# Performance work log

Measured on AMD Instinct MI355X. Metric: run time of the kernel, lower is better.

## Reference

```python
import jax, jax.numpy as jnp
import numpy as np

QK_DIM = 1024
V_DIM = 1024
NUM_HEADS = 16
B, L = 4, 2048


def setup_inputs() -> dict:
    key = jax.random.key(0)
    ks = jax.random.split(key, 12)
    s_in = 1.0 / np.sqrt(QK_DIM)
    inp = {
        "q": jax.random.normal(ks[0], (B, L, QK_DIM), jnp.float32),
        "k": jax.random.normal(ks[1], (B, L, QK_DIM), jnp.float32),
        "v": jax.random.normal(ks[2], (B, L, V_DIM), jnp.float32),
        "Wq": jax.random.uniform(ks[3], (QK_DIM, QK_DIM), jnp.float32, -s_in, s_in),
        "bq": jnp.zeros((QK_DIM,), jnp.float32),
        "Wk": jax.random.uniform(ks[4], (QK_DIM, QK_DIM), jnp.float32, -s_in, s_in),
        "bk": jnp.zeros((QK_DIM,), jnp.float32),
        "Wv": jax.random.uniform(ks[5], (V_DIM, V_DIM), jnp.float32, -s_in, s_in),
        "bv": jnp.zeros((V_DIM,), jnp.float32),
        "Wo": jax.random.uniform(ks[6], (V_DIM, V_DIM), jnp.float32, -s_in, s_in),
        "bo": jnp.zeros((V_DIM,), jnp.float32),
        "offset": jnp.float32(0.0),
    }
    return inp


def _split_heads(x, n_heads):
    b, l, d = x.shape
    return x.reshape(b, l, n_heads, d // n_heads).transpose(0, 2, 1, 3)  # [B,H,L,Dh]


def reference(q, k, v, Wq, bq, Wk, bk, Wv, bv, Wo, bo, offset):
    # in-projections (nn.Linear: x @ W.T + b; here W stored as [in,out])
    q = q @ Wq + bq
    k = k @ Wk + bk
    v = v @ Wv + bv
    scale = (QK_DIM // NUM_HEADS) ** (-0.5)
    q = q * scale
    qh = _split_heads(q, NUM_HEADS)  # [B,H,L,Dh]
    kh = _split_heads(k, NUM_HEADS)
    vh = _split_heads(v, NUM_HEADS)
    scores = jnp.einsum("bhqd,bhkd->bhqk", qh, kh) + offset
    A = jax.nn.softmax(scores, axis=-1)  # attn_dropout is identity in eval
    out = jnp.einsum("bhqk,bhkd->bhqd", A, vh)
    out = out.transpose(0, 2, 1, 3).reshape(B, L, V_DIM)  # merge heads
    out = out @ Wo + bo  # out projection; seq_dropout identity in eval
    return out
```

## Files before the change

kernel.cpp:

```cpp
#include <hip/hip_runtime.h>
#include <hip/hip_bf16.h>
#include <stdint.h>

typedef __bf16 bf16;
typedef __bf16 bf16x8 __attribute__((ext_vector_type(8)));
typedef __bf16 bf16x4v __attribute__((ext_vector_type(4)));
typedef float f32x4 __attribute__((ext_vector_type(4)));
typedef uint32_t u32;
typedef u32 u32x2 __attribute__((ext_vector_type(2)));

__device__ __forceinline__ void gld_lds16(const void* g, void* l) {
  __builtin_amdgcn_global_load_lds(
      (const __attribute__((address_space(1))) void*)g,
      (__attribute__((address_space(3))) void*)l, 16, 0, 0);
}

__device__ __forceinline__ f32x4 mfma16(bf16x8 a, bf16x8 b, f32x4 c) {
  return __builtin_amdgcn_mfma_f32_16x16x32_bf16(a, b, c, 0, 0, 0);
}

__device__ __forceinline__ u32 cvtpk_bf16(float lo, float hi) {
  u32 r;
  asm("v_cvt_pk_bf16_f32 %0, %1, %2" : "=v"(r) : "v"(lo), "v"(hi));
  return r;
}

__device__ __forceinline__ float fexp2(float x) {
#if __has_builtin(__builtin_amdgcn_exp2f)
  return __builtin_amdgcn_exp2f(x);
#else
  return exp2f(x);
#endif
}

__global__ void cvt3_bf16_k(const float* __restrict__ q, const float* __restrict__ k,
                            const float* __restrict__ v, bf16* __restrict__ qb,
                            bf16* __restrict__ kb, bf16* __restrict__ vb, int n4) {
  int i = blockIdx.x * blockDim.x + threadIdx.x;
  if (i >= n4) return;
  const float* in = (blockIdx.y == 0) ? q : (blockIdx.y == 1) ? k : v;
  bf16* out = (blockIdx.y == 0) ? qb : (blockIdx.y == 1) ? kb : vb;
  f32x4 t = reinterpret_cast<const f32x4*>(in)[i];
  bf16x4v o;
  o[0] = (bf16)t[0]; o[1] = (bf16)t[1]; o[2] = (bf16)t[2]; o[3] = (bf16)t[3];
  reinterpret_cast<bf16x4v*>(out)[i] = o;
}

__global__ void wt_cvt4_k(const float* __restrict__ W0, const float* __restrict__ W1,
                          const float* __restrict__ W2, const float* __restrict__ W3,
                          bf16* __restrict__ T0, bf16* __restrict__ T1,
                          bf16* __restrict__ T2, bf16* __restrict__ T3) {
  const float* W = (blockIdx.z == 0) ? W0 : (blockIdx.z == 1) ? W1
                  : (blockIdx.z == 2) ? W2 : W3;
  bf16* WT = (blockIdx.z == 0) ? T0 : (blockIdx.z == 1) ? T1
            : (blockIdx.z == 2) ? T2 : T3;
  __shared__ float t[32][33];
  int tx = threadIdx.x, ty = threadIdx.y;
  int bx = blockIdx.x * 32, by = blockIdx.y * 32;
#pragma unroll
  for (int j = 0; j < 32; j += 8)
    t[ty + j][tx] = W[(size_t)(by + ty + j) * 1024 + bx + tx];
  __syncthreads();
#pragma unroll
  for (int j = 0; j < 32; j += 8)
    WT[(size_t)(bx + ty + j) * 1024 + by + tx] = (bf16)t[tx][ty + j];
}

template <int OUT_MODE>
__global__ __launch_bounds__(256, 2) void gemm_k(
    const bf16* __restrict__ A, const bf16* __restrict__ WT,
    const float* __restrict__ bias, void* __restrict__ Cout, float scale) {
  constexpr int K = 1024, N = 1024, BM = 128, BK = 64;
  constexpr int NT = K / BK;
  __shared__ char lds[2][2][BM * BK * 2];
  const int lane = threadIdx.x & 63, w = threadIdx.x >> 6;
  const int nwg = gridDim.x;
  int bid = (int)blockIdx.x;
  bid = (bid & 7) * (nwg >> 3) + (bid >> 3);
  const int bn = bid & 7;
  const int bm = bid >> 3;
  const int wm = (w & 1) * 64, wn = (w >> 1) * 64;

  const char* gA = (const char*)(A + (size_t)bm * BM * K);
  const char* gB = (const char*)(WT + (size_t)bn * BM * K);

  auto stage = [&](int buf, int kt) {
    char* lA = lds[buf][0];
    char* lB = lds[buf][1];
#pragma unroll
    for (int i = 0; i < 4; ++i) {
      int row = w * 32 + i * 8 + (lane >> 3);
      size_t rb = (size_t)row * (K * 2) + (size_t)kt * (BK * 2) + (size_t)(lane & 7) * 16;
      gld_lds16(gA + rb, lA + (w * 32 + i * 8) * 128);
      gld_lds16(gB + rb, lB + (w * 32 + i * 8) * 128);
    }
  };

  f32x4 acc[4][4] = {};
  stage(0, 0);
  for (int kt = 0; kt < NT; ++kt) {
    __syncthreads();
    if (kt + 1 < NT) stage((kt + 1) & 1, kt + 1);
    const char* lA = lds[kt & 1][0];
    const char* lB = lds[kt & 1][1];
    bf16x8 af[4][2], bfr[4][2];
#pragma unroll
    for (int mi = 0; mi < 4; ++mi)
#pragma unroll
      for (int c = 0; c < 2; ++c) {
        int row = wm + mi * 16 + (lane & 15);
        int ch = c * 4 + (lane >> 4);
        af[mi][c] = *(const bf16x8*)(lA + row * 128 + ch * 16);
      }
#pragma unroll
    for (int ni = 0; ni < 4; ++ni)
#pragma unroll
      for (int c = 0; c < 2; ++c) {
        int row = wn + ni * 16 + (lane & 15);
        int ch = c * 4 + (lane >> 4);
        bfr[ni][c] = *(const bf16x8*)(lB + row * 128 + ch * 16);
      }
#pragma unroll
    for (int mi = 0; mi < 4; ++mi)
#pragma unroll
      for (int ni = 0; ni < 4; ++ni) {
        acc[mi][ni] = mfma16(af[mi][0], bfr[ni][0], acc[mi][ni]);
        acc[mi][ni] = mfma16(af[mi][1], bfr[ni][1], acc[mi][ni]);
      }
  }

#pragma unroll
  for (int ni = 0; ni < 4; ++ni) {
    int col = bn * 128 + wn + ni * 16 + (lane & 15);
    float bv = bias[col];
    if (OUT_MODE == 0) {
      bf16* out = (bf16*)Cout;
      int h = col >> 6, dh = col & 63;
#pragma unroll
      for (int mi = 0; mi < 4; ++mi)
#pragma unroll
        for (int r = 0; r < 4; ++r) {
          int row = bm * BM + wm + mi * 16 + (lane >> 4) * 4 + r;
          int b = row >> 11, li = row & 2047;
          out[(((size_t)(b * 16 + h) * 2048 + li) << 6) + dh] =
              (bf16)((acc[mi][ni][r] + bv) * scale);
        }
    } else if (OUT_MODE == 1) {
      float* out = (float*)Cout;
#pragma unroll
      for (int mi = 0; mi < 4; ++mi)
#pragma unroll
        for (int r = 0; r < 4; ++r) {
          int row = bm * BM + wm + mi * 16 + (lane >> 4) * 4 + r;
          out[(size_t)row * N + col] = acc[mi][ni][r] + bv;
        }
    } else {
      bf16* out = (bf16*)Cout;
      int h = col >> 6, dh = col & 63;
#pragma unroll
      for (int mi = 0; mi < 4; ++mi)
#pragma unroll
        for (int r = 0; r < 4; ++r) {
          int row = bm * BM + wm + mi * 16 + (lane >> 4) * 4 + r;
          int b = row >> 11, li = row & 2047;
          out[(((size_t)(b * 16 + h) * 64 + dh) << 11) + li] =
              (bf16)((acc[mi][ni][r] + bv) * scale);
        }
    }
  }
}

__global__ __launch_bounds__(256, 3) void attn_mfma_k(
    const bf16* __restrict__ Q, const bf16* __restrict__ Kg,
    const bf16* __restrict__ VT, bf16* __restrict__ AO) {
  constexpr int L = 2048, DH = 64, NT = L / 64;
  __shared__ char ldsK[2][8192];
  __shared__ char ldsVT[2][8192];
  __shared__ char ldsP[4][2][2048];
  const int lane = threadIdx.x & 63, w = threadIdx.x >> 6;
  const int nwg = gridDim.x;
  int bid = (int)blockIdx.x;
  bid = (bid & 7) * (nwg >> 3) + (bid >> 3);
  const int bh = bid >> 4;
  const int q0 = (bid & 15) * 128;
  const int b = bh >> 4, h = bh & 15;
  const int l7 = lane & 7;
  const int q15 = lane & 15, g4 = lane >> 4;
  const int sl = lane >> 3;
  const int sw = l7 ^ sl;

  const bf16* Qbase = Q + ((size_t)bh * L + q0 + w * 32) * DH;
  bf16x8 qf[2][2];
#pragma unroll
  for (int rt = 0; rt < 2; ++rt)
#pragma unroll
    for (int c = 0; c < 2; ++c)
      qf[rt][c] = *(const bf16x8*)(Qbase + (size_t)(rt * 16 + q15) * DH +
                                   (c * 4 + g4) * 8);

  const char* Kp  = (const char*)(Kg + (size_t)bh * L * DH);
  const char* VTp = (const char*)(VT + (size_t)bh * DH * L);

  auto stage = [&](int buf, int kt) {
#pragma unroll
    for (int c = 0; c < 2; ++c) {
      int chunk = w * 2 + c;
      int row = chunk * 8 + sl;
      gld_lds16(Kp + (size_t)kt * 8192 + (size_t)row * 128 + sw * 16,
                ldsK[buf] + chunk * 1024);
      gld_lds16(VTp + (size_t)row * 4096 + (size_t)kt * 128 + sw * 16,
                ldsVT[buf] + chunk * 1024);
    }
  };

  f32x4 o[2][4] = {};
  float lpart[2] = {0.f, 0.f};

  stage(0, 0);
  for (int kt = 0; kt < NT; ++kt) {
    __syncthreads();
    if (kt + 1 < NT) stage((kt + 1) & 1, kt + 1);
    const char* lK  = ldsK[kt & 1];
    const char* lVT = ldsVT[kt & 1];

    bf16x8 kf[4][2];
#pragma unroll
    for (int sub = 0; sub < 4; ++sub)
#pragma unroll
      for (int c = 0; c < 2; ++c) {
        int key = sub * 16 + q15;
        int ch = (c * 4 + g4) ^ l7;
        kf[sub][c] = *(const bf16x8*)(lK + key * 128 + ch * 16);
      }

#pragma unroll
    for (int rt = 0; rt < 2; ++rt) {
      f32x4 s[4];
#pragma unroll
      for (int sub = 0; sub < 4; ++sub) {
        f32x4 acc = {};
        acc = mfma16(kf[sub][0], qf[rt][0], acc);
        acc = mfma16(kf[sub][1], qf[rt][1], acc);
        s[sub] = acc;
      }
#pragma unroll
      for (int sub = 0; sub < 4; ++sub) {
        float p0 = fexp2(s[sub][0]), p1 = fexp2(s[sub][1]);
        float p2 = fexp2(s[sub][2]), p3 = fexp2(s[sub][3]);
        lpart[rt] += (p0 + p1) + (p2 + p3);
        u32x2 pw;
        pw[0] = cvtpk_bf16(p0, p1);
        pw[1] = cvtpk_bf16(p2, p3);
        bf16x4v pv = __builtin_bit_cast(bf16x4v, pw);
        int chs = (2 * sub + (g4 >> 1)) ^ l7;
        *(bf16x4v*)(ldsP[w][rt] + q15 * 128 + chs * 16 + (g4 & 1) * 8) = pv;
      }
    }

    asm volatile("s_waitcnt lgkmcnt(0)" ::: "memory");
    __builtin_amdgcn_sched_barrier(0);

    bf16x8 pf[2][2];
#pragma unroll
    for (int rt = 0; rt < 2; ++rt)
#pragma unroll
      for (int c = 0; c < 2; ++c) {
        int ch = (c * 4 + g4) ^ l7;
        pf[rt][c] = *(const bf16x8*)(ldsP[w][rt] + q15 * 128 + ch * 16);
      }

#pragma unroll
    for (int n = 0; n < 4; ++n) {
      int dim = n * 16 + q15;
      bf16x8 vf[2];
#pragma unroll
      for (int c = 0; c < 2; ++c) {
        int ch = (c * 4 + g4) ^ l7;
        vf[c] = *(const bf16x8*)(lVT + dim * 128 + ch * 16);
      }
#pragma unroll
      for (int rt = 0; rt < 2; ++rt) {
        o[rt][n] = mfma16(pf[rt][0], vf[0], o[rt][n]);
        o[rt][n] = mfma16(pf[rt][1], vf[1], o[rt][n]);
      }
    }
  }

  float lf[2];
#pragma unroll
  for (int rt = 0; rt < 2; ++rt) {
    float v = lpart[rt];
    v += __shfl_xor(v, 16, 64);
    v += __shfl_xor(v, 32, 64);
    lf[rt] = v;
  }

#pragma unroll
  for (int rt = 0; rt < 2; ++rt) {
    float inv[4];
#pragma unroll
    for (int r = 0; r < 4; ++r)
      inv[r] = 1.f / __shfl(lf[rt], g4 * 4 + r, 64);
#pragma unroll
    for (int n = 0; n < 4; ++n) {
      int col = h * 64 + n * 16 + q15;
#pragma unroll
      for (int r = 0; r < 4; ++r) {
        int qrow = q0 + w * 32 + rt * 16 + g4 * 4 + r;
        AO[((size_t)b * L + qrow) * 1024 + col] = (bf16)(o[rt][n][r] * inv[r]);
      }
    }
  }
}

extern "C" void kernel_launch(void* const* d_in, const int* in_sizes, int n_in,
                              void* d_out, int out_size, void* d_ws, size_t ws_size,
                              hipStream_t stream) {
  (void)in_sizes; (void)n_in; (void)out_size;
  const size_t MB = 1u << 20;
  if (ws_size < 73 * MB) return;

  const float* q  = (const float*)d_in[0];
  const float* k  = (const float*)d_in[1];
  const float* v  = (const float*)d_in[2];
  const float* Wq = (const float*)d_in[3];
  const float* bq = (const float*)d_in[4];
  const float* Wk = (const float*)d_in[5];
  const float* bk = (const float*)d_in[6];
  const float* Wv = (const float*)d_in[7];
  const float* bv = (const float*)d_in[8];
  const float* Wo = (const float*)d_in[9];
  const float* bo = (const float*)d_in[10];

  char* ws = (char*)d_ws;
  bf16* qb  = (bf16*)(ws + 0 * MB);
  bf16* kb  = (bf16*)(ws + 16 * MB);
  bf16* vb  = (bf16*)(ws + 32 * MB);
  bf16* Qa  = (bf16*)(ws + 48 * MB);
  bf16* WqT = (bf16*)(ws + 64 * MB);
  bf16* WkT = (bf16*)(ws + 66 * MB);
  bf16* WvT = (bf16*)(ws + 68 * MB);
  bf16* WoT = (bf16*)(ws + 70 * MB);
  bf16* Ka = qb;
  bf16* VTa = kb;
  bf16* AO = vb;

  dim3 tb(32, 8);
  wt_cvt4_k<<<dim3(32, 32, 4), tb, 0, stream>>>(Wq, Wk, Wv, Wo, WqT, WkT, WvT, WoT);

  const int n4 = (4 * 2048 * 1024) / 4;
  cvt3_bf16_k<<<dim3(n4 / 256, 3), 256, 0, stream>>>(q, k, v, qb, kb, vb, n4);

  gemm_k<0><<<512, 256, 0, stream>>>(qb, WqT, bq, (void*)Qa, 0.125f * 1.4426950408889634f);
  gemm_k<0><<<512, 256, 0, stream>>>(kb, WkT, bk, (void*)Ka, 1.0f);
  gemm_k<2><<<512, 256, 0, stream>>>(vb, WvT, bv, (void*)VTa, 1.0f);

  attn_mfma_k<<<1024, 256, 0, stream>>>(Qa, Ka, VTa, AO);

  gemm_k<1><<<512, 256, 0, stream>>>(AO, WoT, bo, d_out, 1.0f);
}
```

Before: 215.9 us.

## Fuse fp32-to-bf16 input conversion into batched QKV projection GEMM

Removes the separate pass that converts q/k/v to bf16. The projection GEMM now loads fp32 activations directly, converts them in registers, and writes them swizzled into LDS. The three Q/K/V projection launches are merged into one launch with a grid y-dimension that selects the operand set. This saves a full read and write of the bf16 activation copies plus two launches. In exchange, the A-tile loads become synchronous register loads instead of async global-to-LDS transfers, which may reduce overlap in the main loop.

```diff
diff --git a/kernel.cpp b/kernel.cpp
--- a/kernel.cpp
+++ b/kernel.cpp
@@ -8,6 +8,7 @@
 typedef float f32x4 __attribute__((ext_vector_type(4)));
 typedef uint32_t u32;
 typedef u32 u32x2 __attribute__((ext_vector_type(2)));
+typedef u32 u32x4 __attribute__((ext_vector_type(4)));
 
 __device__ __forceinline__ void gld_lds16(const void* g, void* l) {
   __builtin_amdgcn_global_load_lds(
@@ -31,19 +32,6 @@
 #else
   return exp2f(x);
 #endif
-}
-
-__global__ void cvt3_bf16_k(const float* __restrict__ q, const float* __restrict__ k,
-                            const float* __restrict__ v, bf16* __restrict__ qb,
-                            bf16* __restrict__ kb, bf16* __restrict__ vb, int n4) {
-  int i = blockIdx.x * blockDim.x + threadIdx.x;
-  if (i >= n4) return;
-  const float* in = (blockIdx.y == 0) ? q : (blockIdx.y == 1) ? k : v;
-  bf16* out = (blockIdx.y == 0) ? qb : (blockIdx.y == 1) ? kb : vb;
-  f32x4 t = reinterpret_cast<const f32x4*>(in)[i];
-  bf16x4v o;
-  o[0] = (bf16)t[0]; o[1] = (bf16)t[1]; o[2] = (bf16)t[2]; o[3] = (bf16)t[3];
-  reinterpret_cast<bf16x4v*>(out)[i] = o;
 }
 
 __global__ void wt_cvt4_k(const float* __restrict__ W0, const float* __restrict__ W1,
@@ -66,10 +54,124 @@
     WT[(size_t)(bx + ty + j) * 1024 + by + tx] = (bf16)t[tx][ty + j];
 }
 
-template <int OUT_MODE>
-__global__ __launch_bounds__(256, 2) void gemm_k(
+__global__ __launch_bounds__(256, 2) void gemmf_k(
+    const float* __restrict__ Aq, const float* __restrict__ Ak, const float* __restrict__ Av,
+    const bf16* __restrict__ WTq, const bf16* __restrict__ WTk, const bf16* __restrict__ WTv,
+    const float* __restrict__ bq, const float* __restrict__ bk, const float* __restrict__ bv,
+    bf16* __restrict__ Qa, bf16* __restrict__ Ka, bf16* __restrict__ VTa, float qscale) {
+  constexpr int K = 1024, BM = 128, BK = 64;
+  constexpr int NT = K / BK;
+  __shared__ char lds[2][2][BM * BK * 2];
+  const int lane = threadIdx.x & 63, w = threadIdx.x >> 6;
+  const int y = blockIdx.y;
+  const float* A   = (y == 0) ? Aq : (y == 1) ? Ak : Av;
+  const bf16* WT   = (y == 0) ? WTq : (y == 1) ? WTk : WTv;
+  const float* bias = (y == 0) ? bq : (y == 1) ? bk : bv;
+  const float scale = (y == 0) ? qscale : 1.0f;
+  const int nwg = gridDim.x;
+  int bid = (int)blockIdx.x;
+  bid = (bid & 7) * (nwg >> 3) + (bid >> 3);
+  const int bn = bid & 7;
+  const int bm = bid >> 3;
+  const int wm = (w & 1) * 64, wn = (w >> 1) * 64;
+  const int l7 = lane & 7, sl = lane >> 3;
+  const int sw = l7 ^ sl;
+
+  const char* gA = (const char*)(A + (size_t)bm * BM * K);
+  const char* gB = (const char*)(WT + (size_t)bn * BM * K);
+
+  auto stage = [&](int buf, int kt) {
+    char* lA = lds[buf][0];
+    char* lB = lds[buf][1];
+#pragma unroll
+    for (int i = 0; i < 4; ++i) {
+      int row = w * 32 + i * 8 + sl;
+      size_t rb = (size_t)row * 2048 + (size_t)kt * 128 + (size_t)l7 * 16;
+      gld_lds16(gB + rb, lB + (w * 32 + i * 8) * 128);
+    }
+#pragma unroll
+    for (int i = 0; i < 4; ++i) {
+      int row = w * 32 + i * 8 + sl;
+      const char* src = gA + (size_t)row * 4096 + (size_t)kt * 256 + (size_t)l7 * 32;
+      f32x4 a0 = *(const f32x4*)src;
+      f32x4 a1 = *(const f32x4*)(src + 16);
+      u32x4 pk;
+      pk[0] = cvtpk_bf16(a0[0], a0[1]);
+      pk[1] = cvtpk_bf16(a0[2], a0[3]);
+      pk[2] = cvtpk_bf16(a1[0], a1[1]);
+      pk[3] = cvtpk_bf16(a1[2], a1[3]);
+      bf16x8 v8 = __builtin_bit_cast(bf16x8, pk);
+      *(bf16x8*)(lA + row * 128 + sw * 16) = v8;
+    }
+  };
+
+  f32x4 acc[4][4] = {};
+  stage(0, 0);
+  for (int kt = 0; kt < NT; ++kt) {
+    __syncthreads();
+    if (kt + 1 < NT) stage((kt + 1) & 1, kt + 1);
+    const char* lA = lds[kt & 1][0];
+    const char* lB = lds[kt & 1][1];
+    bf16x8 af[4][2], bfr[4][2];
+#pragma unroll
+    for (int mi = 0; mi < 4; ++mi)
+#pragma unroll
+      for (int c = 0; c < 2; ++c) {
+        int row = wm + mi * 16 + (lane & 15);
+        int ch = (c * 4 + (lane >> 4)) ^ (lane & 7);
+        af[mi][c] = *(const bf16x8*)(lA + row * 128 + ch * 16);
+      }
+#pragma unroll
+    for (int ni = 0; ni < 4; ++ni)
+#pragma unroll
+      for (int c = 0; c < 2; ++c) {
+        int row = wn + ni * 16 + (lane & 15);
+        int ch = c * 4 + (lane >> 4);
+        bfr[ni][c] = *(const bf16x8*)(lB + row * 128 + ch * 16);
+      }
+#pragma unroll
+    for (int mi = 0; mi < 4; ++mi)
+#pragma unroll
+      for (int ni = 0; ni < 4; ++ni) {
+        acc[mi][ni] = mfma16(af[mi][0], bfr[ni][0], acc[mi][ni]);
+        acc[mi][ni] = mfma16(af[mi][1], bfr[ni][1], acc[mi][ni]);
+      }
+  }
+
+#pragma unroll
+  for (int ni = 0; ni < 4; ++ni) {
+    int col = bn * 128 + wn + ni * 16 + (lane & 15);
+    float bv2 = bias[col];
+    int h = col >> 6, dh = col & 63;
+    if (y != 2) {
+      bf16* out = (y == 0) ? Qa : Ka;
+#pragma unroll
+      for (int mi = 0; mi < 4; ++mi)
+#pragma unroll
+        for (int r = 0; r < 4; ++r) {
+          int row = bm * BM + wm + mi * 16 + (lane >> 4) * 4 + r;
+          int b = row >> 11, li = row & 2047;
+          out[(((size_t)(b * 16 + h) * 2048 + li) << 6) + dh] =
+              (bf16)((acc[mi][ni][r] + bv2) * scale);
+        }
+    } else {
+      bf16* out = VTa;
+#pragma unroll
+      for (int mi = 0; mi < 4; ++mi)
+#pragma unroll
+        for (int r = 0; r < 4; ++r) {
+          int row = bm * BM + wm + mi * 16 + (lane >> 4) * 4 + r;
+          int b = row >> 11, li = row & 2047;
+          out[(((size_t)(b * 16 + h) * 64 + dh) << 11) + li] =
+              (bf16)(acc[mi][ni][r] + bv2);
+        }
+    }
+  }
+}
+
+__global__ __launch_bounds__(256, 2) void gemm_out_k(
     const bf16* __restrict__ A, const bf16* __restrict__ WT,
-    const float* __restrict__ bias, void* __restrict__ Cout, float scale) {
+    const float* __restrict__ bias, float* __restrict__ Cout) {
   constexpr int K = 1024, N = 1024, BM = 128, BK = 64;
   constexpr int NT = K / BK;
   __shared__ char lds[2][2][BM * BK * 2];
@@ -133,40 +235,13 @@
   for (int ni = 0; ni < 4; ++ni) {
     int col = bn * 128 + wn + ni * 16 + (lane & 15);
     float bv = bias[col];
-    if (OUT_MODE == 0) {
-      bf16* out = (bf16*)Cout;
-      int h = col >> 6, dh = col & 63;
-#pragma unroll
-      for (int mi = 0; mi < 4; ++mi)
-#pragma unroll
-        for (int r = 0; r < 4; ++r) {
-          int row = bm * BM + wm + mi * 16 + (lane >> 4) * 4 + r;
-          int b = row >> 11, li = row & 2047;
-          out[(((size_t)(b * 16 + h) * 2048 + li) << 6) + dh] =
-              (bf16)((acc[mi][ni][r] + bv) * scale);
-        }
-    } else if (OUT_MODE == 1) {
-      float* out = (float*)Cout;
-#pragma unroll
-      for (int mi = 0; mi < 4; ++mi)
-#pragma unroll
-        for (int r = 0; r < 4; ++r) {
-          int row = bm * BM + wm + mi * 16 + (lane >> 4) * 4 + r;
-          out[(size_t)row * N + col] = acc[mi][ni][r] + bv;
-        }
-    } else {
-      bf16* out = (bf16*)Cout;
-      int h = col >> 6, dh = col & 63;
-#pragma unroll
-      for (int mi = 0; mi < 4; ++mi)
-#pragma unroll
-        for (int r = 0; r < 4; ++r) {
-          int row = bm * BM + wm + mi * 16 + (lane >> 4) * 4 + r;
-          int b = row >> 11, li = row & 2047;
-          out[(((size_t)(b * 16 + h) * 64 + dh) << 11) + li] =
-              (bf16)((acc[mi][ni][r] + bv) * scale);
-        }
-    }
+#pragma unroll
+    for (int mi = 0; mi < 4; ++mi)
+#pragma unroll
+      for (int r = 0; r < 4; ++r) {
+        int row = bm * BM + wm + mi * 16 + (lane >> 4) * 4 + r;
+        Cout[(size_t)row * N + col] = acc[mi][ni][r] + bv;
+      }
   }
 }
 
@@ -333,29 +408,23 @@
   const float* bo = (const float*)d_in[10];
 
   char* ws = (char*)d_ws;
-  bf16* qb  = (bf16*)(ws + 0 * MB);
-  bf16* kb  = (bf16*)(ws + 16 * MB);
-  bf16* vb  = (bf16*)(ws + 32 * MB);
-  bf16* Qa  = (bf16*)(ws + 48 * MB);
+  bf16* Qa  = (bf16*)(ws + 0 * MB);
+  bf16* Ka  = (bf16*)(ws + 16 * MB);
+  bf16* VTa = (bf16*)(ws + 32 * MB);
+  bf16* AO  = (bf16*)(ws + 48 * MB);
   bf16* WqT = (bf16*)(ws + 64 * MB);
   bf16* WkT = (bf16*)(ws + 66 * MB);
   bf16* WvT = (bf16*)(ws + 68 * MB);
   bf16* WoT = (bf16*)(ws + 70 * MB);
-  bf16* Ka = qb;
-  bf16* VTa = kb;
-  bf16* AO = vb;
 
   dim3 tb(32, 8);
   wt_cvt4_k<<<dim3(32, 32, 4), tb, 0, stream>>>(Wq, Wk, Wv, Wo, WqT, WkT, WvT, WoT);
 
-  const int n4 = (4 * 2048 * 1024) / 4;
-  cvt3_bf16_k<<<dim3(n4 / 256, 3), 256, 0, stream>>>(q, k, v, qb, kb, vb, n4);
-
-  gemm_k<0><<<512, 256, 0, stream>>>(qb, WqT, bq, (void*)Qa, 0.125f * 1.4426950408889634f);
-  gemm_k<0><<<512, 256, 0, stream>>>(kb, WkT, bk, (void*)Ka, 1.0f);
-  gemm_k<2><<<512, 256, 0, stream>>>(vb, WvT, bv, (void*)VTa, 1.0f);
+  gemmf_k<<<dim3(512, 3), 256, 0, stream>>>(
+      q, k, v, WqT, WkT, WvT, bq, bk, bv, Qa, Ka, VTa,
+      0.125f * 1.4426950408889634f);
 
   attn_mfma_k<<<1024, 256, 0, stream>>>(Qa, Ka, VTa, AO);
 
-  gemm_k<1><<<512, 256, 0, stream>>>(AO, WoT, bo, d_out, 1.0f);
-}
+  gemm_out_k<<<512, 256, 0, stream>>>(AO, WoT, bo, (float*)d_out);
+}
```

Measured after the change: 205.8 us. 4.7% less time.
